# Kernel tuning notes

Measured on AMD Instinct MI355X. Metric: run time of the kernel, lower is better.

## Reference

```python
import jax, jax.numpy as jnp
import numpy as np

B, L, D = 64, 2048, 60
P, PS = 16, 30  # num patches, patch size

def setup_inputs() -> dict:
    key = jax.random.key(0)
    k1, k2, k3, k4 = jax.random.split(key, 4)
    seq1M = jax.random.normal(k1, (B, L, D), dtype=jnp.float32)
    seq2M = jax.random.normal(k2, (B, L, D), dtype=jnp.float32)
    geo = jax.random.normal(k3, (B, P, PS, PS), dtype=jnp.float32)
    patches = jax.random.randint(k4, (B, P, 2), 0, L - PS, dtype=jnp.int32)
    return {"seq1M": seq1M, "seq2M": seq2M, "geo": geo, "patches": patches}

def reference(seq1M, seq2M, geo, patches):
    # rows: seq1M[b, patches[b,p,0] : +PS, :] -> [B,P,PS,D]
    # cols: seq2M[b, patches[b,p,1] : +PS, :] -> [B,P,PS,D]
    offs = jnp.arange(PS)  # [PS]
    bidx = jnp.arange(seq1M.shape[0])[:, None, None]  # [B,1,1]
    ridx = patches[:, :, 0][..., None] + offs  # [B,P,PS]
    cidx = patches[:, :, 1][..., None] + offs  # [B,P,PS]
    rows = seq1M[bidx, ridx]  # [B,P,PS,D]
    cols = seq2M[bidx, cidx]  # [B,P,PS,D]
    # block[b,p,a,c] = concat(rows[b,p,c], cols[b,p,a], geo[b,p,a,c])
    shp = rows.shape[:2] + (PS, PS, rows.shape[-1])  # [B,P,PS,PS,D]
    row_t = jnp.broadcast_to(rows[:, :, None, :, :], shp)
    col_t = jnp.broadcast_to(cols[:, :, :, None, :], shp)
    return jnp.concatenate([row_t, col_t, geo[..., None]], axis=-1)  # [B,P,PS,PS,2D+1]
```

## Files before the change

kernel.cpp:

```cpp
#include <hip/hip_runtime.h>


constexpr int B_    = 64;
constexpr int L_    = 2048;
constexpr int D_    = 60;
constexpr int P_    = 16;
constexpr int PS_   = 30;
constexpr int KOUT  = 2 * D_ + 1;
constexpr int NPAIR = PS_ * PS_;
constexpr int CHUNK = NPAIR * KOUT;
constexpr int SPLIT = 2;
constexpr int NT    = 256;
constexpr int WAVES_PER_CHUNK = SPLIT * (NT / 64);

__global__ __launch_bounds__(NT) void make_blocks_38860864094557_kernel(
    const float* __restrict__ seq1, const float* __restrict__ seq2,
    const float* __restrict__ geo,  const int* __restrict__ patches,
    float* __restrict__ out)
{
    __shared__ float sh_rows[PS_ * D_];
    __shared__ float sh_cols[PS_ * D_];
    __shared__ float sh_geo [NPAIR];

    const int bid = blockIdx.x;
    const int bp  = bid / SPLIT;
    const int s   = bid % SPLIT;
    const int b   = bp / P_;

    const int r0 = patches[bp * 2 + 0];
    const int c0 = patches[bp * 2 + 1];

    const float4* rsrc = reinterpret_cast<const float4*>(seq1 + ((size_t)b * L_ + r0) * D_);
    const float4* csrc = reinterpret_cast<const float4*>(seq2 + ((size_t)b * L_ + c0) * D_);
    const float4* gsrc = reinterpret_cast<const float4*>(geo  + (size_t)bp * NPAIR);

    for (int i = threadIdx.x; i < PS_ * D_ / 4; i += NT) {
        reinterpret_cast<float4*>(sh_rows)[i] = rsrc[i];
        reinterpret_cast<float4*>(sh_cols)[i] = csrc[i];
    }
    for (int i = threadIdx.x; i < NPAIR / 4; i += NT) {
        reinterpret_cast<float4*>(sh_geo)[i] = gsrc[i];
    }
    __syncthreads();

    const int lane = threadIdx.x & 63;
    const int wid  = threadIdx.x >> 6;
    const int gw   = s * (NT / 64) + wid;

    float* chunk = out + (size_t)bp * CHUNK;

    for (int q = gw; q < NPAIR; q += WAVES_PER_CHUNK) {
        const int a = q / PS_;
        const int c = q - a * PS_;
        float* dst = chunk + q * KOUT;

        if (lane < D_) dst[lane] = sh_rows[c * D_ + lane];

        const float v = (lane < D_) ? sh_cols[a * D_ + lane] : sh_geo[q];
        if (lane < D_ + 1) dst[D_ + lane] = v;
    }
}

extern "C" void kernel_launch(void* const* d_in, const int* in_sizes, int n_in,
                              void* d_out, int out_size, void* d_ws, size_t ws_size,
                              hipStream_t stream) {
    const float* seq1    = (const float*)d_in[0];
    const float* seq2    = (const float*)d_in[1];
    const float* geo     = (const float*)d_in[2];
    const int*   patches = (const int*)d_in[3];
    float*       out     = (float*)d_out;

    const int grid = B_ * P_ * SPLIT;
    make_blocks_38860864094557_kernel<<<grid, NT, 0, stream>>>(seq1, seq2, geo, patches, out);
}
```

Baseline: 128.4 us.

## Write output as coalesced float4 stores via precomputed padded LDS offsets

Changes the write path so each thread emits contiguous float4 chunks of the output. Each chunk covers two 'a' rows at a time, and the thread's LDS gather offsets and strides are precomputed once in registers. Row and column staging in LDS is padded to 61 floats to reduce bank conflicts. The launch uses one 512-thread block per patch instead of two 256-thread blocks, removing the scalar, partially masked 121-wide stores. The trade-offs are more registers per thread, scalar staging loads, and half as many blocks.

```diff
diff --git a/kernel.cpp b/kernel.cpp
--- a/kernel.cpp
+++ b/kernel.cpp
@@ -9,55 +9,88 @@
 constexpr int KOUT  = 2 * D_ + 1;
 constexpr int NPAIR = PS_ * PS_;
 constexpr int CHUNK = NPAIR * KOUT;
-constexpr int SPLIT = 2;
-constexpr int NT    = 256;
-constexpr int WAVES_PER_CHUNK = SPLIT * (NT / 64);
+constexpr int AP_FLOATS = 2 * PS_ * KOUT;
+constexpr int AP_F4     = AP_FLOATS / 4;
+constexpr int NAP       = PS_ / 2;
+
+constexpr int NT = 512;
+constexpr int NS = (AP_F4 + NT - 1) / NT;
+
+constexpr int RPAD = 61;
+constexpr int CB   = PS_ * RPAD;
+constexpr int GB   = CB + PS_ * RPAD;
+constexpr int LDSF = GB + NPAIR;
 
 __global__ __launch_bounds__(NT) void make_blocks_38860864094557_kernel(
     const float* __restrict__ seq1, const float* __restrict__ seq2,
     const float* __restrict__ geo,  const int* __restrict__ patches,
     float* __restrict__ out)
 {
-    __shared__ float sh_rows[PS_ * D_];
-    __shared__ float sh_cols[PS_ * D_];
-    __shared__ float sh_geo [NPAIR];
+    __shared__ float sh[LDSF];
 
-    const int bid = blockIdx.x;
-    const int bp  = bid / SPLIT;
-    const int s   = bid % SPLIT;
-    const int b   = bp / P_;
+    const int bp = blockIdx.x;
+    const int b  = bp / P_;
+    const int tid = threadIdx.x;
 
     const int r0 = patches[bp * 2 + 0];
     const int c0 = patches[bp * 2 + 1];
 
-    const float4* rsrc = reinterpret_cast<const float4*>(seq1 + ((size_t)b * L_ + r0) * D_);
-    const float4* csrc = reinterpret_cast<const float4*>(seq2 + ((size_t)b * L_ + c0) * D_);
-    const float4* gsrc = reinterpret_cast<const float4*>(geo  + (size_t)bp * NPAIR);
+    const float* s1 = seq1 + ((size_t)b * L_ + r0) * D_;
+    const float* s2 = seq2 + ((size_t)b * L_ + c0) * D_;
+    const float* gg = geo  + (size_t)bp * NPAIR;
 
-    for (int i = threadIdx.x; i < PS_ * D_ / 4; i += NT) {
-        reinterpret_cast<float4*>(sh_rows)[i] = rsrc[i];
-        reinterpret_cast<float4*>(sh_cols)[i] = csrc[i];
+    for (int i = tid; i < PS_ * RPAD; i += NT) {
+        const int c  = i / RPAD;
+        const int kk = i - c * RPAD;
+        if (kk < D_) {
+            sh[i]      = s1[c * D_ + kk];
+            sh[CB + i] = s2[c * D_ + kk];
+        }
     }
-    for (int i = threadIdx.x; i < NPAIR / 4; i += NT) {
-        reinterpret_cast<float4*>(sh_geo)[i] = gsrc[i];
-    }
+    for (int i = tid; i < NPAIR; i += NT) sh[GB + i] = gg[i];
     __syncthreads();
 
-    const int lane = threadIdx.x & 63;
-    const int wid  = threadIdx.x >> 6;
-    const int gw   = s * (NT / 64) + wid;
+    int offb[NS][4];
+    int strb[NS][4];
+    bool valid[NS];
+#pragma unroll
+    for (int s = 0; s < NS; ++s) {
+        const int u4 = tid + s * NT;
+        valid[s] = (u4 < AP_F4);
+        const int u4c = valid[s] ? u4 : (AP_F4 - 1);
+#pragma unroll
+        for (int j = 0; j < 4; ++j) {
+            const int u  = 4 * u4c + j;
+            const int ah = (u >= PS_ * KOUT) ? 1 : 0;
+            const int r  = u - ah * PS_ * KOUT;
+            const int c  = r / KOUT;
+            const int k  = r - c * KOUT;
+            int off, st;
+            if (k < D_)            { off = c * RPAD + k;               st = 0; }
+            else if (k < 2 * D_)   { off = CB + ah * RPAD + (k - D_);  st = 2 * RPAD; }
+            else                   { off = GB + ah * PS_ + c;          st = 2 * PS_; }
+            offb[s][j] = off * 4;
+            strb[s][j] = st * 4;
+        }
+    }
 
-    float* chunk = out + (size_t)bp * CHUNK;
+    float4* outf4 = reinterpret_cast<float4*>(out + (size_t)bp * CHUNK);
+    const char* shb = reinterpret_cast<const char*>(sh);
 
-    for (int q = gw; q < NPAIR; q += WAVES_PER_CHUNK) {
-        const int a = q / PS_;
-        const int c = q - a * PS_;
-        float* dst = chunk + q * KOUT;
-
-        if (lane < D_) dst[lane] = sh_rows[c * D_ + lane];
-
-        const float v = (lane < D_) ? sh_cols[a * D_ + lane] : sh_geo[q];
-        if (lane < D_ + 1) dst[D_ + lane] = v;
+    for (int ap = 0; ap < NAP; ++ap) {
+#pragma unroll
+        for (int s = 0; s < NS; ++s) {
+            if (valid[s]) {
+                float4 v;
+                v.x = *reinterpret_cast<const float*>(shb + offb[s][0]);
+                v.y = *reinterpret_cast<const float*>(shb + offb[s][1]);
+                v.z = *reinterpret_cast<const float*>(shb + offb[s][2]);
+                v.w = *reinterpret_cast<const float*>(shb + offb[s][3]);
+                outf4[ap * AP_F4 + tid + s * NT] = v;
+            }
+#pragma unroll
+            for (int j = 0; j < 4; ++j) offb[s][j] += strb[s][j];
+        }
     }
 }
 
@@ -70,6 +103,6 @@
     const int*   patches = (const int*)d_in[3];
     float*       out     = (float*)d_out;
 
-    const int grid = B_ * P_ * SPLIT;
+    const int grid = B_ * P_;
     make_blocks_38860864094557_kernel<<<grid, NT, 0, stream>>>(seq1, seq2, geo, patches, out);
 }
```

New measurement: 113.0 us. 1.14x faster.
